# Kernel tuning notes

Hardware: AMD Instinct MI355X
Metric: run time of the kernel (lower is better)

Reference implementation:

```python
import jax, jax.numpy as jnp
import numpy as np

HEADS, DHEAD = 8, 32
INNER = HEADS * DHEAD  # 256


def _conv3x3(x, w, b):
    y = jax.lax.conv_general_dilated(x, w, (1, 1), ((1, 1), (1, 1)),
                                     dimension_numbers=('NCHW', 'OIHW', 'NCHW'))
    return y + b[None, :, None, None]


def _conv1x1(x, w, b):
    return jnp.einsum('oc,bchw->bohw', w, x) + b[None, :, None, None]


def setup_inputs() -> dict:
    key = jax.random.key(0)
    ks = jax.random.split(key, 16)
    s = 0.02
    return {
        'x': jax.random.normal(ks[0], (2, 256, 48, 48), jnp.float32),
        'luma': jax.random.uniform(ks[1], (2, 1, 48, 48), jnp.float32),
        'w_qkv': jax.random.normal(ks[2], (768, 256), jnp.float32) * s,
        'b_qkv': jax.random.normal(ks[3], (768,), jnp.float32) * s,
        'w_proj': jax.random.normal(ks[4], (256, 256), jnp.float32) * s,
        'b_proj': jax.random.normal(ks[5], (256,), jnp.float32) * s,
        'w_c1': jax.random.normal(ks[6], (128, 1, 3, 3), jnp.float32) * s,
        'b_c1': jax.random.normal(ks[7], (128,), jnp.float32) * s,
        'w_c2': jax.random.normal(ks[8], (128, 128, 3, 3), jnp.float32) * s,
        'b_c2': jax.random.normal(ks[9], (128,), jnp.float32) * s,
        'w_g': jax.random.normal(ks[10], (256, 128), jnp.float32) * s,
        'b_g': jax.random.normal(ks[11], (256,), jnp.float32) * s,
        'w_bt': jax.random.normal(ks[12], (256, 128), jnp.float32) * s,
        'b_bt': jax.random.normal(ks[13], (256,), jnp.float32) * s,
        'alpha': jax.random.normal(ks[14], (), jnp.float32) * 0.1,
    }


def reference(x, luma, w_qkv, b_qkv, w_proj, b_proj, w_c1, b_c1, w_c2, b_c2,
              w_g, b_g, w_bt, b_bt, alpha):
    B, C, H, W = x.shape
    N = H * W
    scale = DHEAD ** -0.5

    def to_heads(t):  # [B, h*d, H, W] -> [B, h, N, d]
        return t.reshape(B, HEADS, DHEAD, N).transpose(0, 1, 3, 2)

    qkv = _conv1x1(x, w_qkv, b_qkv)
    q = to_heads(qkv[:, 0 * INNER:1 * INNER])
    k = to_heads(qkv[:, 1 * INNER:2 * INNER])
    v = to_heads(qkv[:, 2 * INNER:3 * INNER])

    # luma conditioning net
    h = jax.nn.relu(_conv3x3(luma, w_c1, b_c1))
    h = jax.nn.relu(_conv3x3(h, w_c2, b_c2))
    gamma = to_heads(_conv1x1(h, w_g, b_g))
    beta = to_heads(_conv1x1(h, w_bt, b_bt))
    q = gamma * q + beta
    k = gamma * k + beta
    v = gamma * v + beta

    # luminance bias: avg_pool2d(3, stride=1, pad=1, count_include_pad=True)
    invL = 1.0 - luma
    invL = jax.lax.reduce_window(invL, 0.0, jax.lax.add, (1, 1, 3, 3), (1, 1, 1, 1),
                                 ((0, 0), (0, 0), (1, 1), (1, 1))) / 9.0
    invL = invL.reshape(B, N)
    invL = invL - invL.mean(axis=-1, keepdims=True)
    q = q + alpha * invL[:, None, :, None]

    attn = jax.nn.softmax(jnp.einsum('bhid,bhjd->bhij', q, k) * scale, axis=-1)
    out = jnp.einsum('bhij,bhjd->bhid', attn, v)
    out = out.transpose(0, 1, 3, 2).reshape(B, INNER, H, W)
    return _conv1x1(out, w_proj, b_proj)
```

## Files before the change

### kernel.cpp

```cpp
#include <hip/hip_runtime.h>
#include <hip/hip_bf16.h>
#include <math.h>
#include <string.h>

#define NB 2
#define NN 2304
#define NHEADS 8
#define DH 32
#define KPW 576

typedef __attribute__((ext_vector_type(8))) short v8s;
typedef __attribute__((ext_vector_type(4))) float v4f;

__device__ inline unsigned short f2b(float f) {
    unsigned u = __builtin_bit_cast(unsigned, f);
    unsigned r = u + 0x7FFFu + ((u >> 16) & 1u);
    return (unsigned short)(r >> 16);
}
__device__ inline float b2f(short s) {
    unsigned u = ((unsigned)(unsigned short)s) << 16;
    return __builtin_bit_cast(float, u);
}
__device__ inline unsigned pk2(float a, float b) {
    __hip_bfloat162 h = __float22bfloat162_rn(make_float2(a, b));
    unsigned r;
    memcpy(&r, &h, sizeof(r));
    return r;
}
__device__ inline float blo(unsigned u) { return __builtin_bit_cast(float, u << 16); }
__device__ inline float bhi(unsigned u) { return __builtin_bit_cast(float, u & 0xffff0000u); }

__global__ void k_prep(const float* __restrict__ wc1, const float* __restrict__ wc2,
                       const float* __restrict__ wqkv, const float* __restrict__ wg,
                       const float* __restrict__ wbt, const float* __restrict__ wproj,
                       float* __restrict__ twc1, short* __restrict__ tc2b,
                       short* __restrict__ wqkvb, short* __restrict__ wgb,
                       short* __restrict__ wbtb, short* __restrict__ wprojb,
                       float* __restrict__ vsum) {
    int i = blockIdx.x * 256 + threadIdx.x;
    if (i < 16 * DH) vsum[i] = 0.f;
    if (i < 9 * 128) {
        int k = i / 128, c = i % 128;
        twc1[i] = wc1[c * 9 + k];
    }
    if (i < 9 * 128 * 128) {
        int s = i / (128 * 128);
        int rem = i % (128 * 128);
        int o = rem / 128, ic = rem % 128;
        tc2b[i] = (short)f2b(wc2[(o * 128 + ic) * 9 + s]);
    }
    if (i < 768 * 256) wqkvb[i] = (short)f2b(wqkv[i]);
    if (i < 256 * 128) { wgb[i] = (short)f2b(wg[i]); wbtb[i] = (short)f2b(wbt[i]); }
    if (i < 256 * 256) wprojb[i] = (short)f2b(wproj[i]);
}

__global__ void k_front(const float* __restrict__ x, short* __restrict__ xt,
                        const float* __restrict__ luma, float* __restrict__ invl,
                        const float* __restrict__ twc1, const float* __restrict__ bc1,
                        short* __restrict__ h1p) {
    __shared__ unsigned short lds[64 * 66];
    __shared__ float red[256];
    int blk = blockIdx.x;
    if (blk >= NB * 144 + NB) {
        int cb = blk - (NB * 144 + NB);
        int c = threadIdx.x & 127;
        int p = (cb % 1250) * 2 + (threadIdx.x >> 7);
        int b = cb / 1250;
        int py = p / 50, px = p % 50;
        float val = 0.f;
        if (py >= 1 && py <= 48 && px >= 1 && px <= 48) {
            int y = py - 1, xx0 = px - 1;
            const float* lb = luma + b * NN;
            float acc = bc1[c];
#pragma unroll
            for (int ky = 0; ky < 3; ++ky) {
                int yy = y + ky - 1;
                if (yy < 0 || yy >= 48) continue;
#pragma unroll
                for (int kx = 0; kx < 3; ++kx) {
                    int xx = xx0 + kx - 1;
                    if (xx < 0 || xx >= 48) continue;
                    acc += twc1[(ky * 3 + kx) * 128 + c] * lb[yy * 48 + xx];
                }
            }
            val = fmaxf(acc, 0.f);
        }
        h1p[((size_t)b * 2500 + p) * 128 + c] = (short)f2b(val);
        return;
    }
    if (blk >= NB * 144) {
        int b = blk - NB * 144;
        const float* lb = luma + b * NN;
        float pooled[9];
        float local = 0.f;
#pragma unroll
        for (int it = 0; it < 9; ++it) {
            int n = it * 256 + threadIdx.x;
            int y = n / 48, xx0 = n % 48;
            float s = 0.f;
            for (int ky = 0; ky < 3; ++ky) {
                int yy = y + ky - 1;
                if (yy < 0 || yy >= 48) continue;
                for (int kx = 0; kx < 3; ++kx) {
                    int xx = xx0 + kx - 1;
                    if (xx < 0 || xx >= 48) continue;
                    s += 1.f - lb[yy * 48 + xx];
                }
            }
            s *= (1.f / 9.f);
            pooled[it] = s;
            local += s;
        }
        red[threadIdx.x] = local;
        __syncthreads();
        for (int off = 128; off > 0; off >>= 1) {
            if (threadIdx.x < off) red[threadIdx.x] += red[threadIdx.x + off];
            __syncthreads();
        }
        float mean = red[0] * (1.f / NN);
#pragma unroll
        for (int it = 0; it < 9; ++it) {
            int n = it * 256 + threadIdx.x;
            invl[b * NN + n] = pooled[it] - mean;
        }
        return;
    }
    int nt = blk % 36, ct = (blk / 36) % 4, b = blk / 144;
    int n0 = nt * 64, c0 = ct * 64;
    int nc = threadIdx.x & 63, cr = threadIdx.x >> 6;
#pragma unroll
    for (int i = 0; i < 16; ++i) {
        int cs = i * 4 + cr;
        float v = x[((size_t)b * 256 + c0 + cs) * NN + n0 + nc];
        lds[nc * 66 + cs] = f2b(v);
    }
    __syncthreads();
    int cc = threadIdx.x & 31, nr = threadIdx.x >> 5;
    unsigned* xt2 = (unsigned*)xt;
#pragma unroll
    for (int j = 0; j < 8; ++j) {
        int ns = j * 8 + nr;
        unsigned w = *(unsigned*)&lds[ns * 66 + 2 * cc];
        xt2[(((size_t)b * NN + n0 + ns) * 256 + c0) / 2 + cc] = w;
    }
}

__global__ __launch_bounds__(64) void k_conv2m(const short* __restrict__ h1p,
                                               const short* __restrict__ tc2b,
                                               const float* __restrict__ bc2,
                                               short* __restrict__ h2t) {
    int lane = threadIdx.x, l15 = lane & 15, g = lane >> 4;
    int blk = blockIdx.x;
    int ntg = blk % 36, ot = (blk / 36) % 8, b = blk / (36 * 8);
    int p0[4], na[4];
#pragma unroll
    for (int j = 0; j < 4; ++j) {
        int nt = ntg * 4 + j;
        int y = nt / 3, xx = (nt % 3) * 16;
        p0[j] = (y + 1) * 50 + xx + 1;
        na[j] = y * 48 + xx + l15;
    }
    const short* hb = h1p + (size_t)b * 2500 * 128;

    v4f acc[4] = {{0.f,0.f,0.f,0.f},{0.f,0.f,0.f,0.f},{0.f,0.f,0.f,0.f},{0.f,0.f,0.f,0.f}};
#pragma unroll
    for (int s = 0; s < 9; ++s) {
        int dp = (s / 3 - 1) * 50 + (s % 3 - 1);
#pragma unroll
        for (int kk = 0; kk < 4; ++kk) {
            v8s A = *(const v8s*)(tc2b + ((size_t)(s * 128 + ot * 16 + l15)) * 128 + kk * 32 + 8 * g);
#pragma unroll
            for (int j = 0; j < 4; ++j) {
                v8s B = *(const v8s*)(hb + (size_t)(p0[j] + dp + l15) * 128 + kk * 32 + 8 * g);
                acc[j] = __builtin_amdgcn_mfma_f32_16x16x32_bf16(A, B, acc[j], 0, 0, 0);
            }
        }
    }
    v4f bias = *(const v4f*)&bc2[ot * 16 + 4 * g];
#pragma unroll
    for (int j = 0; j < 4; ++j) {
        uint2 w;
        w.x = pk2(fmaxf(acc[j][0] + bias[0], 0.f), fmaxf(acc[j][1] + bias[1], 0.f));
        w.y = pk2(fmaxf(acc[j][2] + bias[2], 0.f), fmaxf(acc[j][3] + bias[3], 0.f));
        *(uint2*)&h2t[((size_t)b * NN + na[j]) * 128 + ot * 16 + 4 * g] = w;
    }
}

__global__ __launch_bounds__(64) void k_gbm(const short* __restrict__ h2t,
                                            const short* __restrict__ wgb,
                                            const short* __restrict__ wbtb,
                                            const float* __restrict__ bg,
                                            const float* __restrict__ bbt,
                                            short* __restrict__ gtb, short* __restrict__ bttb) {
    int lane = threadIdx.x, l15 = lane & 15, g = lane >> 4;
    int blk = blockIdx.x;
    int ntg = blk % 36, ot = (blk / 36) % 16, b = blk / (36 * 16);
    int n0 = ntg * 64;
    const short* hb = h2t + (size_t)b * NN * 128;

    v4f ga[4] = {{0.f,0.f,0.f,0.f},{0.f,0.f,0.f,0.f},{0.f,0.f,0.f,0.f},{0.f,0.f,0.f,0.f}};
    v4f ta[4] = {{0.f,0.f,0.f,0.f},{0.f,0.f,0.f,0.f},{0.f,0.f,0.f,0.f},{0.f,0.f,0.f,0.f}};
#pragma unroll
    for (int kk = 0; kk < 4; ++kk) {
        v8s Ag = *(const v8s*)(wgb + (size_t)(ot * 16 + l15) * 128 + kk * 32 + 8 * g);
        v8s At = *(const v8s*)(wbtb + (size_t)(ot * 16 + l15) * 128 + kk * 32 + 8 * g);
#pragma unroll
        for (int j = 0; j < 4; ++j) {
            v8s B = *(const v8s*)(hb + (size_t)(n0 + j * 16 + l15) * 128 + kk * 32 + 8 * g);
            ga[j] = __builtin_amdgcn_mfma_f32_16x16x32_bf16(Ag, B, ga[j], 0, 0, 0);
            ta[j] = __builtin_amdgcn_mfma_f32_16x16x32_bf16(At, B, ta[j], 0, 0, 0);
        }
    }
    v4f bgv = *(const v4f*)&bg[ot * 16 + 4 * g];
    v4f bbv = *(const v4f*)&bbt[ot * 16 + 4 * g];
#pragma unroll
    for (int j = 0; j < 4; ++j) {
        size_t o = ((size_t)b * NN + n0 + j * 16 + l15) * 256 + ot * 16 + 4 * g;
        uint2 w;
        w.x = pk2(ga[j][0] + bgv[0], ga[j][1] + bgv[1]);
        w.y = pk2(ga[j][2] + bgv[2], ga[j][3] + bgv[3]);
        *(uint2*)&gtb[o] = w;
        w.x = pk2(ta[j][0] + bbv[0], ta[j][1] + bbv[1]);
        w.y = pk2(ta[j][2] + bbv[2], ta[j][3] + bbv[3]);
        *(uint2*)&bttb[o] = w;
    }
}

__global__ __launch_bounds__(64) void k_qkvm(const short* __restrict__ xt,
                                             const short* __restrict__ wqkvb,
                                             const float* __restrict__ bqkv,
                                             const short* __restrict__ gtb,
                                             const short* __restrict__ bttb,
                                             const float* __restrict__ invl,
                                             const float* __restrict__ alpha_p,
                                             short* __restrict__ qb, short* __restrict__ kb,
                                             short* __restrict__ vraw) {
    int lane = threadIdx.x, l15 = lane & 15, g = lane >> 4;
    int blk = blockIdx.x;
    int ntg = blk % 36, otg = (blk / 36) % 24, b = blk / (36 * 24);
    int n0 = ntg * 64;
    const short* xb = xt + (size_t)b * NN * 256;

    v4f acc[2][4];
#pragma unroll
    for (int oa = 0; oa < 2; ++oa)
#pragma unroll
        for (int j = 0; j < 4; ++j) acc[oa][j] = (v4f){0.f, 0.f, 0.f, 0.f};
#pragma unroll
    for (int kk = 0; kk < 8; ++kk) {
        v8s A0 = *(const v8s*)(wqkvb + (size_t)(otg * 32 + l15) * 256 + kk * 32 + 8 * g);
        v8s A1 = *(const v8s*)(wqkvb + (size_t)(otg * 32 + 16 + l15) * 256 + kk * 32 + 8 * g);
#pragma unroll
        for (int j = 0; j < 4; ++j) {
            v8s B = *(const v8s*)(xb + (size_t)(n0 + j * 16 + l15) * 256 + kk * 32 + 8 * g);
            acc[0][j] = __builtin_amdgcn_mfma_f32_16x16x32_bf16(A0, B, acc[0][j], 0, 0, 0);
            acc[1][j] = __builtin_amdgcn_mfma_f32_16x16x32_bf16(A1, B, acc[1][j], 0, 0, 0);
        }
    }
    const float scale = 0.25503486f;
    float alpha = *alpha_p;
#pragma unroll
    for (int oa = 0; oa < 2; ++oa) {
        int ocb = otg * 32 + oa * 16;
        int which = ocb >> 8;
        int cbase = (ocb & 255) + 4 * g;
        int h = cbase >> 5, dbase = cbase & 31;
        v4f bias = *(const v4f*)&bqkv[ocb + 4 * g];
        short* dst = (which == 0) ? qb : (which == 1) ? kb : vraw;
#pragma unroll
        for (int j = 0; j < 4; ++j) {
            int n = n0 + j * 16 + l15;
            v4f a = acc[oa][j];
            uint2 gg = *(const uint2*)&gtb[((size_t)b * NN + n) * 256 + cbase];
            uint2 tt = *(const uint2*)&bttb[((size_t)b * NN + n) * 256 + cbase];
            float iv = (which == 0) ? alpha * invl[b * NN + n] : 0.f;
            float v0 = blo(gg.x) * (a[0] + bias[0]) + blo(tt.x);
            float v1 = bhi(gg.x) * (a[1] + bias[1]) + bhi(tt.x);
            float v2 = blo(gg.y) * (a[2] + bias[2]) + blo(tt.y);
            float v3 = bhi(gg.y) * (a[3] + bias[3]) + bhi(tt.y);
            if (which == 0) {
                v0 = (v0 + iv) * scale; v1 = (v1 + iv) * scale;
                v2 = (v2 + iv) * scale; v3 = (v3 + iv) * scale;
            }
            uint2 w;
            w.x = pk2(v0, v1);
            w.y = pk2(v2, v3);
            *(uint2*)&dst[(((size_t)b * NHEADS + h) * NN + n) * DH + dbase] = w;
        }
    }
}

__global__ void k_vt(const short* __restrict__ vraw, short* __restrict__ vtb,
                     float* __restrict__ vsum) {
    __shared__ unsigned short lds[64 * 34];
    int bh = blockIdx.x / 36, nc = blockIdx.x % 36;
    int n0 = nc * 64;
    int dpair = threadIdx.x & 15, nsub = (threadIdx.x >> 4) & 15;
    const unsigned* vr2 = (const unsigned*)vraw;
#pragma unroll
    for (int i = 0; i < 4; ++i) {
        int ns = i * 16 + nsub;
        unsigned v = vr2[((size_t)bh * NN + n0 + ns) * 16 + dpair];
        *(unsigned*)&lds[ns * 34 + 2 * dpair] = v;
    }
    __syncthreads();
    int pn = threadIdx.x & 31, drow = threadIdx.x >> 5;
    int kb0 = n0 >> 5;
    unsigned* vtb2 = (unsigned*)vtb;
#pragma unroll
    for (int j = 0; j < 4; ++j) {
        int d = j * 8 + drow;
        unsigned lo = lds[(2 * pn) * 34 + d];
        unsigned hi = lds[(2 * pn + 1) * 34 + d];
        vtb2[(((size_t)bh * 72 + kb0 + (pn >> 4)) * 32 + d) * 16 + (pn & 15)] = lo | (hi << 16);
    }
    if (threadIdx.x < 32) {
        int d = threadIdx.x;
        float s = 0.f;
        for (int ns = 0; ns < 64; ++ns) s += b2f((short)lds[ns * 34 + d]);
        atomicAdd(&vsum[bh * DH + d], s);
    }
}

__global__ __launch_bounds__(256) void k_attn2(const short* __restrict__ qb,
                                               const short* __restrict__ kbuf,
                                               const short* __restrict__ vtb,
                                               const float* __restrict__ vsum,
                                               short* __restrict__ aotb) {
    __shared__ short plds[4][64 * 40];
    __shared__ float acc_lds[4][64][35];
    __shared__ float ps_lds[4][64];
    int tid = threadIdx.x;
    int w = tid >> 6, lane = tid & 63;
    int l15 = lane & 15, g = lane >> 4;
    int blk = blockIdx.x;
    int logical = (blk & 7) * 72 + (blk >> 3);
    int qt = logical % 36, bh = logical / 36;
    int qbase = qt * 64;

    const short* qp = qb + ((size_t)bh * NN + qbase) * DH;
    const short* kp = kbuf + ((size_t)bh * NN + w * KPW) * DH;
    const short* vp = vtb + ((size_t)bh * 72 + w * (KPW / 32)) * 1024;

    v8s q0 = *(const v8s*)(qp + l15 * DH + 8 * g);
    v8s q1 = *(const v8s*)(qp + (16 + l15) * DH + 8 * g);
    v8s q2 = *(const v8s*)(qp + (32 + l15) * DH + 8 * g);
    v8s q3 = *(const v8s*)(qp + (48 + l15) * DH + 8 * g);

    const short one_b = (short)0x3F80;
    const v8s ones = {one_b, one_b, one_b, one_b, one_b, one_b, one_b, one_b};

    v4f acc[2][4];
#pragma unroll
    for (int dt = 0; dt < 2; ++dt)
#pragma unroll
        for (int qf = 0; qf < 4; ++qf) acc[dt][qf] = (v4f){0.f, 0.f, 0.f, 0.f};
    v4f ps[4] = {{0.f,0.f,0.f,0.f},{0.f,0.f,0.f,0.f},{0.f,0.f,0.f,0.f},{0.f,0.f,0.f,0.f}};
    short* pw = plds[w];

    for (int it = 0; it < KPW / 32; ++it) {
        const short* kpi = kp + it * 32 * DH;
        v8s ka0 = *(const v8s*)(kpi + l15 * DH + 8 * g);
        v8s ka1 = *(const v8s*)(kpi + (16 + l15) * DH + 8 * g);
        v4f s00 = __builtin_amdgcn_mfma_f32_16x16x32_bf16(ka0, q0, (v4f){0.f,0.f,0.f,0.f}, 0, 0, 0);
        v4f s01 = __builtin_amdgcn_mfma_f32_16x16x32_bf16(ka0, q1, (v4f){0.f,0.f,0.f,0.f}, 0, 0, 0);
        v4f s02 = __builtin_amdgcn_mfma_f32_16x16x32_bf16(ka0, q2, (v4f){0.f,0.f,0.f,0.f}, 0, 0, 0);
        v4f s03 = __builtin_amdgcn_mfma_f32_16x16x32_bf16(ka0, q3, (v4f){0.f,0.f,0.f,0.f}, 0, 0, 0);
        v4f s10 = __builtin_amdgcn_mfma_f32_16x16x32_bf16(ka1, q0, (v4f){0.f,0.f,0.f,0.f}, 0, 0, 0);
        v4f s11 = __builtin_amdgcn_mfma_f32_16x16x32_bf16(ka1, q1, (v4f){0.f,0.f,0.f,0.f}, 0, 0, 0);
        v4f s12 = __builtin_amdgcn_mfma_f32_16x16x32_bf16(ka1, q2, (v4f){0.f,0.f,0.f,0.f}, 0, 0, 0);
        v4f s13 = __builtin_amdgcn_mfma_f32_16x16x32_bf16(ka1, q3, (v4f){0.f,0.f,0.f,0.f}, 0, 0, 0);

#define DOFRAG(S, QF, KT)                                                        \
        {                                                                        \
            float p0 = __builtin_amdgcn_exp2f((S)[0]) - 1.f;                     \
            float p1 = __builtin_amdgcn_exp2f((S)[1]) - 1.f;                     \
            float p2 = __builtin_amdgcn_exp2f((S)[2]) - 1.f;                     \
            float p3 = __builtin_amdgcn_exp2f((S)[3]) - 1.f;                     \
            uint2 wv;                                                            \
            wv.x = pk2(p0, p1);                                                  \
            wv.y = pk2(p2, p3);                                                  \
            *(uint2*)((char*)pw + ((QF) * 16 + l15) * 80 + ((KT) * 16 + 4 * g) * 2) = wv; \
        }
        DOFRAG(s00, 0, 0)
        DOFRAG(s01, 1, 0)
        DOFRAG(s02, 2, 0)
        DOFRAG(s03, 3, 0)
        DOFRAG(s10, 0, 1)
        DOFRAG(s11, 1, 1)
        DOFRAG(s12, 2, 1)
        DOFRAG(s13, 3, 1)
#undef DOFRAG
        v8s pa0 = *(v8s*)((char*)pw + l15 * 80 + 16 * g);
        v8s pa1 = *(v8s*)((char*)pw + (16 + l15) * 80 + 16 * g);
        v8s pa2 = *(v8s*)((char*)pw + (32 + l15) * 80 + 16 * g);
        v8s pa3 = *(v8s*)((char*)pw + (48 + l15) * 80 + 16 * g);
        const short* vpi = vp + it * 1024;
        v8s vb0 = *(const v8s*)(vpi + l15 * 32 + 8 * g);
        v8s vb1 = *(const v8s*)(vpi + (16 + l15) * 32 + 8 * g);
        __builtin_amdgcn_s_setprio(1);
        acc[0][0] = __builtin_amdgcn_mfma_f32_16x16x32_bf16(pa0, vb0, acc[0][0], 0, 0, 0);
        acc[1][0] = __builtin_amdgcn_mfma_f32_16x16x32_bf16(pa0, vb1, acc[1][0], 0, 0, 0);
        acc[0][1] = __builtin_amdgcn_mfma_f32_16x16x32_bf16(pa1, vb0, acc[0][1], 0, 0, 0);
        acc[1][1] = __builtin_amdgcn_mfma_f32_16x16x32_bf16(pa1, vb1, acc[1][1], 0, 0, 0);
        acc[0][2] = __builtin_amdgcn_mfma_f32_16x16x32_bf16(pa2, vb0, acc[0][2], 0, 0, 0);
        acc[1][2] = __builtin_amdgcn_mfma_f32_16x16x32_bf16(pa2, vb1, acc[1][2], 0, 0, 0);
        acc[0][3] = __builtin_amdgcn_mfma_f32_16x16x32_bf16(pa3, vb0, acc[0][3], 0, 0, 0);
        acc[1][3] = __builtin_amdgcn_mfma_f32_16x16x32_bf16(pa3, vb1, acc[1][3], 0, 0, 0);
        ps[0] = __builtin_amdgcn_mfma_f32_16x16x32_bf16(pa0, ones, ps[0], 0, 0, 0);
        ps[1] = __builtin_amdgcn_mfma_f32_16x16x32_bf16(pa1, ones, ps[1], 0, 0, 0);
        ps[2] = __builtin_amdgcn_mfma_f32_16x16x32_bf16(pa2, ones, ps[2], 0, 0, 0);
        ps[3] = __builtin_amdgcn_mfma_f32_16x16x32_bf16(pa3, ones, ps[3], 0, 0, 0);
        __builtin_amdgcn_s_setprio(0);
    }

    if (l15 == 0) {
#pragma unroll
        for (int qf = 0; qf < 4; ++qf)
#pragma unroll
            for (int r = 0; r < 4; ++r)
                ps_lds[w][qf * 16 + 4 * g + r] = ps[qf][r];
    }
#pragma unroll
    for (int qf = 0; qf < 4; ++qf)
#pragma unroll
        for (int dt = 0; dt < 2; ++dt)
#pragma unroll
            for (int r = 0; r < 4; ++r)
                acc_lds[w][qf * 16 + 4 * g + r][dt * 16 + l15] = acc[dt][qf][r];
    __syncthreads();

    int q = tid >> 2, d0 = (tid & 3) * 8;
    float L = (float)NN;
    float a[8] = {0.f, 0.f, 0.f, 0.f, 0.f, 0.f, 0.f, 0.f};
#pragma unroll
    for (int wv = 0; wv < 4; ++wv) {
        L += ps_lds[wv][q];
        const float* row = &acc_lds[wv][q][d0];
#pragma unroll
        for (int j = 0; j < 8; ++j) a[j] += row[j];
    }
    const float* vs = vsum + bh * DH + d0;
    float rl = 1.f / L;
    uint4 o;
    o.x = pk2((a[0] + vs[0]) * rl, (a[1] + vs[1]) * rl);
    o.y = pk2((a[2] + vs[2]) * rl, (a[3] + vs[3]) * rl);
    o.z = pk2((a[4] + vs[4]) * rl, (a[5] + vs[5]) * rl);
    o.w = pk2((a[6] + vs[6]) * rl, (a[7] + vs[7]) * rl);
    int b = bh >> 3, h = bh & 7;
    *(uint4*)&aotb[((size_t)b * NN + qbase + q) * 256 + h * DH + d0] = o;
}

__global__ __launch_bounds__(64) void k_projm(const short* __restrict__ aotb,
                                              const short* __restrict__ wprojb,
                                              const float* __restrict__ bproj,
                                              float* __restrict__ out) {
    int lane = threadIdx.x, l15 = lane & 15, g = lane >> 4;
    int blk = blockIdx.x;
    int ntg = blk % 36, otg = (blk / 36) % 8, b = blk / (36 * 8);
    int n0 = ntg * 64;
    const short* ab = aotb + (size_t)b * NN * 256;

    v4f acc[2][4];
#pragma unroll
    for (int oa = 0; oa < 2; ++oa)
#pragma unroll
        for (int j = 0; j < 4; ++j) acc[oa][j] = (v4f){0.f, 0.f, 0.f, 0.f};
#pragma unroll
    for (int kk = 0; kk < 8; ++kk) {
        v8s A0 = *(const v8s*)(wprojb + (size_t)(otg * 32 + l15) * 256 + kk * 32 + 8 * g);
        v8s A1 = *(const v8s*)(wprojb + (size_t)(otg * 32 + 16 + l15) * 256 + kk * 32 + 8 * g);
#pragma unroll
        for (int j = 0; j < 4; ++j) {
            v8s B = *(const v8s*)(ab + (size_t)(n0 + j * 16 + l15) * 256 + kk * 32 + 8 * g);
            acc[0][j] = __builtin_amdgcn_mfma_f32_16x16x32_bf16(A0, B, acc[0][j], 0, 0, 0);
            acc[1][j] = __builtin_amdgcn_mfma_f32_16x16x32_bf16(A1, B, acc[1][j], 0, 0, 0);
        }
    }
#pragma unroll
    for (int oa = 0; oa < 2; ++oa) {
        v4f bias = *(const v4f*)&bproj[otg * 32 + oa * 16 + 4 * g];
#pragma unroll
        for (int j = 0; j < 4; ++j) {
#pragma unroll
            for (int r = 0; r < 4; ++r) {
                int o = otg * 32 + oa * 16 + 4 * g + r;
                out[((size_t)b * 256 + o) * NN + n0 + j * 16 + l15] = acc[oa][j][r] + bias[r];
            }
        }
    }
}

extern "C" void kernel_launch(void* const* d_in, const int* in_sizes, int n_in,
                              void* d_out, int out_size, void* d_ws, size_t ws_size,
                              hipStream_t stream) {
    const float* x     = (const float*)d_in[0];
    const float* luma  = (const float*)d_in[1];
    const float* wqkv  = (const float*)d_in[2];
    const float* bqkv  = (const float*)d_in[3];
    const float* wproj = (const float*)d_in[4];
    const float* bproj = (const float*)d_in[5];
    const float* wc1   = (const float*)d_in[6];
    const float* bc1   = (const float*)d_in[7];
    const float* wc2   = (const float*)d_in[8];
    const float* bc2   = (const float*)d_in[9];
    const float* wg    = (const float*)d_in[10];
    const float* bg    = (const float*)d_in[11];
    const float* wbt   = (const float*)d_in[12];
    const float* bbt   = (const float*)d_in[13];
    const float* alpha = (const float*)d_in[14];
    float* out = (float*)d_out;

    float* ws = (float*)d_ws;
    size_t off = 0;
    float* twc1 = ws + off;            off += 9 * 128;
    short* tc2b = (short*)(ws + off);  off += 9 * 128 * 128 / 2;
    short* wqkvb = (short*)(ws + off); off += 768 * 256 / 2;
    short* wgb = (short*)(ws + off);   off += 256 * 128 / 2;
    short* wbtb = (short*)(ws + off);  off += 256 * 128 / 2;
    short* wprojb = (short*)(ws + off); off += 256 * 256 / 2;
    short* h1p = (short*)(ws + off);   off += NB * 2500 * 128 / 2;
    short* xt = (short*)(ws + off);    off += NB * NN * 256 / 2;
    short* h2t = (short*)(ws + off);   off += NB * NN * 128 / 2;
    short* gtb = (short*)(ws + off);   off += NB * NN * 256 / 2;
    short* bttb = (short*)(ws + off);  off += NB * NN * 256 / 2;
    float* invl = ws + off;            off += NB * NN;
    short* qbb = (short*)(ws + off);   off += 16 * NN * DH / 2;
    short* kbb = (short*)(ws + off);   off += 16 * NN * DH / 2;
    short* vraw = (short*)(ws + off);  off += 16 * NN * DH / 2;
    short* vtb = (short*)(ws + off);   off += 16 * NN * DH / 2;
    float* vsum = ws + off;            off += 16 * DH;
    short* aotb = (short*)(ws + off);  off += NB * NN * 256 / 2;
    (void)ws_size; (void)in_sizes; (void)n_in; (void)out_size;

    k_prep<<<768, 256, 0, stream>>>(wc1, wc2, wqkv, wg, wbt, wproj,
                                    twc1, tc2b, wqkvb, wgb, wbtb, wprojb, vsum);
    k_front<<<NB * 144 + NB + NB * 1250, 256, 0, stream>>>(x, xt, luma, invl, twc1, bc1, h1p);
    k_conv2m<<<NB * 8 * 36, 64, 0, stream>>>(h1p, tc2b, bc2, h2t);
    k_gbm<<<NB * 16 * 36, 64, 0, stream>>>(h2t, wgb, wbtb, bg, bbt, gtb, bttb);
    k_qkvm<<<NB * 24 * 36, 64, 0, stream>>>(xt, wqkvb, bqkv, gtb, bttb, invl, alpha,
                                            qbb, kbb, vraw);
    k_vt<<<16 * 36, 256, 0, stream>>>(vraw, vtb, vsum);
    k_attn2<<<576, 256, 0, stream>>>(qbb, kbb, vtb, vsum, aotb);
    k_projm<<<NB * 8 * 36, 64, 0, stream>>>(aotb, wprojb, bproj, out);
}
```

Measured before the change: 111.0 us.

## Split attention into 32-query tiles with 8 key-split waves per block

The attention kernel now gives each block 32 queries instead of 64 and splits the keys across 8 waves of 288 keys rather than 4 waves of 576. Grid and block sizes double, which raises parallelism and shortens each wave's serial loop. The cross-wave partial sums now pass through LDS as bf16 instead of fp32, which shrinks shared memory but adds rounding error. Q-fragment reuse per K/V load is halved, so global K/V traffic per query roughly doubles.

New measurement: 98.57 us. -11.2%, faster.

```diff
diff --git a/kernel.cpp b/kernel.cpp
--- a/kernel.cpp
+++ b/kernel.cpp
@@ -7,7 +7,8 @@
 #define NN 2304
 #define NHEADS 8
 #define DH 32
-#define KPW 576
+#define AW 8
+#define KPW 288
 
 typedef __attribute__((ext_vector_type(8))) short v8s;
 typedef __attribute__((ext_vector_type(4))) float v4f;
@@ -322,21 +323,21 @@
     }
 }
 
-__global__ __launch_bounds__(256) void k_attn2(const short* __restrict__ qb,
+__global__ __launch_bounds__(512) void k_attn2(const short* __restrict__ qb,
                                                const short* __restrict__ kbuf,
                                                const short* __restrict__ vtb,
                                                const float* __restrict__ vsum,
                                                short* __restrict__ aotb) {
-    __shared__ short plds[4][64 * 40];
-    __shared__ float acc_lds[4][64][35];
-    __shared__ float ps_lds[4][64];
+    __shared__ short plds[AW][32 * 40];
+    __shared__ short acch[AW][32][33];
+    __shared__ float ps_lds[AW][32];
     int tid = threadIdx.x;
     int w = tid >> 6, lane = tid & 63;
     int l15 = lane & 15, g = lane >> 4;
     int blk = blockIdx.x;
-    int logical = (blk & 7) * 72 + (blk >> 3);
-    int qt = logical % 36, bh = logical / 36;
-    int qbase = qt * 64;
+    int logical = (blk & 7) * 144 + (blk >> 3);
+    int qt = logical % 72, bh = logical / 72;
+    int qbase = qt * 32;
 
     const short* qp = qb + ((size_t)bh * NN + qbase) * DH;
     const short* kp = kbuf + ((size_t)bh * NN + w * KPW) * DH;
@@ -344,18 +345,12 @@
 
     v8s q0 = *(const v8s*)(qp + l15 * DH + 8 * g);
     v8s q1 = *(const v8s*)(qp + (16 + l15) * DH + 8 * g);
-    v8s q2 = *(const v8s*)(qp + (32 + l15) * DH + 8 * g);
-    v8s q3 = *(const v8s*)(qp + (48 + l15) * DH + 8 * g);
 
     const short one_b = (short)0x3F80;
     const v8s ones = {one_b, one_b, one_b, one_b, one_b, one_b, one_b, one_b};
 
-    v4f acc[2][4];
-#pragma unroll
-    for (int dt = 0; dt < 2; ++dt)
-#pragma unroll
-        for (int qf = 0; qf < 4; ++qf) acc[dt][qf] = (v4f){0.f, 0.f, 0.f, 0.f};
-    v4f ps[4] = {{0.f,0.f,0.f,0.f},{0.f,0.f,0.f,0.f},{0.f,0.f,0.f,0.f},{0.f,0.f,0.f,0.f}};
+    v4f acc00 = {0.f,0.f,0.f,0.f}, acc01 = acc00, acc10 = acc00, acc11 = acc00;
+    v4f ps0 = {0.f,0.f,0.f,0.f}, ps1 = ps0;
     short* pw = plds[w];
 
     for (int it = 0; it < KPW / 32; ++it) {
@@ -364,12 +359,8 @@
         v8s ka1 = *(const v8s*)(kpi + (16 + l15) * DH + 8 * g);
         v4f s00 = __builtin_amdgcn_mfma_f32_16x16x32_bf16(ka0, q0, (v4f){0.f,0.f,0.f,0.f}, 0, 0, 0);
         v4f s01 = __builtin_amdgcn_mfma_f32_16x16x32_bf16(ka0, q1, (v4f){0.f,0.f,0.f,0.f}, 0, 0, 0);
-        v4f s02 = __builtin_amdgcn_mfma_f32_16x16x32_bf16(ka0, q2, (v4f){0.f,0.f,0.f,0.f}, 0, 0, 0);
-        v4f s03 = __builtin_amdgcn_mfma_f32_16x16x32_bf16(ka0, q3, (v4f){0.f,0.f,0.f,0.f}, 0, 0, 0);
         v4f s10 = __builtin_amdgcn_mfma_f32_16x16x32_bf16(ka1, q0, (v4f){0.f,0.f,0.f,0.f}, 0, 0, 0);
         v4f s11 = __builtin_amdgcn_mfma_f32_16x16x32_bf16(ka1, q1, (v4f){0.f,0.f,0.f,0.f}, 0, 0, 0);
-        v4f s12 = __builtin_amdgcn_mfma_f32_16x16x32_bf16(ka1, q2, (v4f){0.f,0.f,0.f,0.f}, 0, 0, 0);
-        v4f s13 = __builtin_amdgcn_mfma_f32_16x16x32_bf16(ka1, q3, (v4f){0.f,0.f,0.f,0.f}, 0, 0, 0);
 
 #define DOFRAG(S, QF, KT)                                                        \
         {                                                                        \
@@ -384,71 +375,54 @@
         }
         DOFRAG(s00, 0, 0)
         DOFRAG(s01, 1, 0)
-        DOFRAG(s02, 2, 0)
-        DOFRAG(s03, 3, 0)
         DOFRAG(s10, 0, 1)
         DOFRAG(s11, 1, 1)
-        DOFRAG(s12, 2, 1)
-        DOFRAG(s13, 3, 1)
 #undef DOFRAG
         v8s pa0 = *(v8s*)((char*)pw + l15 * 80 + 16 * g);
         v8s pa1 = *(v8s*)((char*)pw + (16 + l15) * 80 + 16 * g);
-        v8s pa2 = *(v8s*)((char*)pw + (32 + l15) * 80 + 16 * g);
-        v8s pa3 = *(v8s*)((char*)pw + (48 + l15) * 80 + 16 * g);
         const short* vpi = vp + it * 1024;
         v8s vb0 = *(const v8s*)(vpi + l15 * 32 + 8 * g);
         v8s vb1 = *(const v8s*)(vpi + (16 + l15) * 32 + 8 * g);
         __builtin_amdgcn_s_setprio(1);
-        acc[0][0] = __builtin_amdgcn_mfma_f32_16x16x32_bf16(pa0, vb0, acc[0][0], 0, 0, 0);
-        acc[1][0] = __builtin_amdgcn_mfma_f32_16x16x32_bf16(pa0, vb1, acc[1][0], 0, 0, 0);
-        acc[0][1] = __builtin_amdgcn_mfma_f32_16x16x32_bf16(pa1, vb0, acc[0][1], 0, 0, 0);
-        acc[1][1] = __builtin_amdgcn_mfma_f32_16x16x32_bf16(pa1, vb1, acc[1][1], 0, 0, 0);
-        acc[0][2] = __builtin_amdgcn_mfma_f32_16x16x32_bf16(pa2, vb0, acc[0][2], 0, 0, 0);
-        acc[1][2] = __builtin_amdgcn_mfma_f32_16x16x32_bf16(pa2, vb1, acc[1][2], 0, 0, 0);
-        acc[0][3] = __builtin_amdgcn_mfma_f32_16x16x32_bf16(pa3, vb0, acc[0][3], 0, 0, 0);
-        acc[1][3] = __builtin_amdgcn_mfma_f32_16x16x32_bf16(pa3, vb1, acc[1][3], 0, 0, 0);
-        ps[0] = __builtin_amdgcn_mfma_f32_16x16x32_bf16(pa0, ones, ps[0], 0, 0, 0);
-        ps[1] = __builtin_amdgcn_mfma_f32_16x16x32_bf16(pa1, ones, ps[1], 0, 0, 0);
-        ps[2] = __builtin_amdgcn_mfma_f32_16x16x32_bf16(pa2, ones, ps[2], 0, 0, 0);
-        ps[3] = __builtin_amdgcn_mfma_f32_16x16x32_bf16(pa3, ones, ps[3], 0, 0, 0);
+        acc00 = __builtin_amdgcn_mfma_f32_16x16x32_bf16(pa0, vb0, acc00, 0, 0, 0);
+        acc01 = __builtin_amdgcn_mfma_f32_16x16x32_bf16(pa0, vb1, acc01, 0, 0, 0);
+        acc10 = __builtin_amdgcn_mfma_f32_16x16x32_bf16(pa1, vb0, acc10, 0, 0, 0);
+        acc11 = __builtin_amdgcn_mfma_f32_16x16x32_bf16(pa1, vb1, acc11, 0, 0, 0);
+        ps0 = __builtin_amdgcn_mfma_f32_16x16x32_bf16(pa0, ones, ps0, 0, 0, 0);
+        ps1 = __builtin_amdgcn_mfma_f32_16x16x32_bf16(pa1, ones, ps1, 0, 0, 0);
         __builtin_amdgcn_s_setprio(0);
     }
 
     if (l15 == 0) {
 #pragma unroll
-        for (int qf = 0; qf < 4; ++qf)
-#pragma unroll
-            for (int r = 0; r < 4; ++r)
-                ps_lds[w][qf * 16 + 4 * g + r] = ps[qf][r];
-    }
-#pragma unroll
-    for (int qf = 0; qf < 4; ++qf)
-#pragma unroll
-        for (int dt = 0; dt < 2; ++dt)
-#pragma unroll
-            for (int r = 0; r < 4; ++r)
-                acc_lds[w][qf * 16 + 4 * g + r][dt * 16 + l15] = acc[dt][qf][r];
+        for (int r = 0; r < 4; ++r) {
+            ps_lds[w][4 * g + r] = ps0[r];
+            ps_lds[w][16 + 4 * g + r] = ps1[r];
+        }
+    }
+#pragma unroll
+    for (int r = 0; r < 4; ++r) {
+        acch[w][4 * g + r][l15]      = (short)f2b(acc00[r]);
+        acch[w][4 * g + r][16 + l15] = (short)f2b(acc01[r]);
+        acch[w][16 + 4 * g + r][l15]      = (short)f2b(acc10[r]);
+        acch[w][16 + 4 * g + r][16 + l15] = (short)f2b(acc11[r]);
+    }
     __syncthreads();
 
-    int q = tid >> 2, d0 = (tid & 3) * 8;
+    int q = tid >> 4, d0 = (tid & 15) * 2;
     float L = (float)NN;
-    float a[8] = {0.f, 0.f, 0.f, 0.f, 0.f, 0.f, 0.f, 0.f};
-#pragma unroll
-    for (int wv = 0; wv < 4; ++wv) {
+    float a0 = 0.f, a1 = 0.f;
+#pragma unroll
+    for (int wv = 0; wv < AW; ++wv) {
         L += ps_lds[wv][q];
-        const float* row = &acc_lds[wv][q][d0];
-#pragma unroll
-        for (int j = 0; j < 8; ++j) a[j] += row[j];
+        a0 += b2f(acch[wv][q][d0]);
+        a1 += b2f(acch[wv][q][d0 + 1]);
     }
     const float* vs = vsum + bh * DH + d0;
     float rl = 1.f / L;
-    uint4 o;
-    o.x = pk2((a[0] + vs[0]) * rl, (a[1] + vs[1]) * rl);
-    o.y = pk2((a[2] + vs[2]) * rl, (a[3] + vs[3]) * rl);
-    o.z = pk2((a[4] + vs[4]) * rl, (a[5] + vs[5]) * rl);
-    o.w = pk2((a[6] + vs[6]) * rl, (a[7] + vs[7]) * rl);
+    unsigned o = pk2((a0 + vs[0]) * rl, (a1 + vs[1]) * rl);
     int b = bh >> 3, h = bh & 7;
-    *(uint4*)&aotb[((size_t)b * NN + qbase + q) * 256 + h * DH + d0] = o;
+    *(unsigned*)&aotb[((size_t)b * NN + qbase + q) * 256 + h * DH + d0] = o;
 }
 
 __global__ __launch_bounds__(64) void k_projm(const short* __restrict__ aotb,
@@ -541,6 +515,6 @@
     k_qkvm<<<NB * 24 * 36, 64, 0, stream>>>(xt, wqkvb, bqkv, gtb, bttb, invl, alpha,
                                             qbb, kbb, vraw);
     k_vt<<<16 * 36, 256, 0, stream>>>(vraw, vtb, vsum);
-    k_attn2<<<576, 256, 0, stream>>>(qbb, kbb, vtb, vsum, aotb);
+    k_attn2<<<1152, 512, 0, stream>>>(qbb, kbb, vtb, vsum, aotb);
     k_projm<<<NB * 8 * 36, 64, 0, stream>>>(aotb, wprojb, bproj, out);
 }
```

## Fold weight prep into front kernel and split attention keys over eight waves

Applied to the files above, without the earlier changes.

Weight conversion to bf16 now runs as extra blocks of the front kernel, and the conv1 weights are read directly instead of through a transposed copy. This removes one kernel launch and its serialization. The attention kernel now uses 8 waves (512 threads), each covering 288 keys instead of 576, which doubles parallelism within a block. The per-wave partial accumulators are stored in LDS as bf16 so the larger wave count still fits in shared memory. That adds rounding error to the partial sums before they are reduced.

Result: faster. 98.71 us (-11.1%).

```diff
diff --git a/kernel.cpp b/kernel.cpp
--- a/kernel.cpp
+++ b/kernel.cpp
@@ -7,7 +7,8 @@
 #define NN 2304
 #define NHEADS 8
 #define DH 32
-#define KPW 576
+#define AW 8
+#define KPW 288
 
 typedef __attribute__((ext_vector_type(8))) short v8s;
 typedef __attribute__((ext_vector_type(4))) float v4f;
@@ -30,39 +31,38 @@
 __device__ inline float blo(unsigned u) { return __builtin_bit_cast(float, u << 16); }
 __device__ inline float bhi(unsigned u) { return __builtin_bit_cast(float, u & 0xffff0000u); }
 
-__global__ void k_prep(const float* __restrict__ wc1, const float* __restrict__ wc2,
-                       const float* __restrict__ wqkv, const float* __restrict__ wg,
-                       const float* __restrict__ wbt, const float* __restrict__ wproj,
-                       float* __restrict__ twc1, short* __restrict__ tc2b,
-                       short* __restrict__ wqkvb, short* __restrict__ wgb,
-                       short* __restrict__ wbtb, short* __restrict__ wprojb,
-                       float* __restrict__ vsum) {
-    int i = blockIdx.x * 256 + threadIdx.x;
-    if (i < 16 * DH) vsum[i] = 0.f;
-    if (i < 9 * 128) {
-        int k = i / 128, c = i % 128;
-        twc1[i] = wc1[c * 9 + k];
-    }
-    if (i < 9 * 128 * 128) {
-        int s = i / (128 * 128);
-        int rem = i % (128 * 128);
-        int o = rem / 128, ic = rem % 128;
-        tc2b[i] = (short)f2b(wc2[(o * 128 + ic) * 9 + s]);
-    }
-    if (i < 768 * 256) wqkvb[i] = (short)f2b(wqkv[i]);
-    if (i < 256 * 128) { wgb[i] = (short)f2b(wg[i]); wbtb[i] = (short)f2b(wbt[i]); }
-    if (i < 256 * 256) wprojb[i] = (short)f2b(wproj[i]);
-}
-
 __global__ void k_front(const float* __restrict__ x, short* __restrict__ xt,
                         const float* __restrict__ luma, float* __restrict__ invl,
-                        const float* __restrict__ twc1, const float* __restrict__ bc1,
-                        short* __restrict__ h1p) {
+                        const float* __restrict__ wc1, const float* __restrict__ bc1,
+                        short* __restrict__ h1p,
+                        const float* __restrict__ wc2, const float* __restrict__ wqkv,
+                        const float* __restrict__ wg, const float* __restrict__ wbt,
+                        const float* __restrict__ wproj,
+                        short* __restrict__ tc2b, short* __restrict__ wqkvb,
+                        short* __restrict__ wgb, short* __restrict__ wbtb,
+                        short* __restrict__ wprojb, float* __restrict__ vsum) {
     __shared__ unsigned short lds[64 * 66];
     __shared__ float red[256];
     int blk = blockIdx.x;
-    if (blk >= NB * 144 + NB) {
-        int cb = blk - (NB * 144 + NB);
+    const int XT_END = NB * 144;
+    const int INVL_END = XT_END + NB;
+    const int CONV1_END = INVL_END + NB * 1250;
+    if (blk >= CONV1_END) {
+        int i = (blk - CONV1_END) * 256 + threadIdx.x;
+        if (i < 16 * DH) vsum[i] = 0.f;
+        if (i < 9 * 128 * 128) {
+            int s = i / (128 * 128);
+            int rem = i % (128 * 128);
+            int o = rem / 128, ic = rem % 128;
+            tc2b[i] = (short)f2b(wc2[(o * 128 + ic) * 9 + s]);
+        }
+        if (i < 768 * 256) wqkvb[i] = (short)f2b(wqkv[i]);
+        if (i < 256 * 128) { wgb[i] = (short)f2b(wg[i]); wbtb[i] = (short)f2b(wbt[i]); }
+        if (i < 256 * 256) wprojb[i] = (short)f2b(wproj[i]);
+        return;
+    }
+    if (blk >= INVL_END) {
+        int cb = blk - INVL_END;
         int c = threadIdx.x & 127;
         int p = (cb % 1250) * 2 + (threadIdx.x >> 7);
         int b = cb / 1250;
@@ -80,7 +80,7 @@
                 for (int kx = 0; kx < 3; ++kx) {
                     int xx = xx0 + kx - 1;
                     if (xx < 0 || xx >= 48) continue;
-                    acc += twc1[(ky * 3 + kx) * 128 + c] * lb[yy * 48 + xx];
+                    acc += wc1[c * 9 + ky * 3 + kx] * lb[yy * 48 + xx];
                 }
             }
             val = fmaxf(acc, 0.f);
@@ -88,8 +88,8 @@
         h1p[((size_t)b * 2500 + p) * 128 + c] = (short)f2b(val);
         return;
     }
-    if (blk >= NB * 144) {
-        int b = blk - NB * 144;
+    if (blk >= XT_END) {
+        int b = blk - XT_END;
         const float* lb = luma + b * NN;
         float pooled[9];
         float local = 0.f;
@@ -322,14 +322,14 @@
     }
 }
 
-__global__ __launch_bounds__(256) void k_attn2(const short* __restrict__ qb,
+__global__ __launch_bounds__(512) void k_attn2(const short* __restrict__ qb,
                                                const short* __restrict__ kbuf,
                                                const short* __restrict__ vtb,
                                                const float* __restrict__ vsum,
                                                short* __restrict__ aotb) {
-    __shared__ short plds[4][64 * 40];
-    __shared__ float acc_lds[4][64][35];
-    __shared__ float ps_lds[4][64];
+    __shared__ short plds[AW][64 * 40];
+    __shared__ short acch[AW][64][36];
+    __shared__ float ps_lds[AW][64];
     int tid = threadIdx.x;
     int w = tid >> 6, lane = tid & 63;
     int l15 = lane & 15, g = lane >> 4;
@@ -424,31 +424,28 @@
 #pragma unroll
     for (int qf = 0; qf < 4; ++qf)
 #pragma unroll
-        for (int dt = 0; dt < 2; ++dt)
-#pragma unroll
-            for (int r = 0; r < 4; ++r)
-                acc_lds[w][qf * 16 + 4 * g + r][dt * 16 + l15] = acc[dt][qf][r];
+        for (int r = 0; r < 4; ++r) {
+            acch[w][qf * 16 + 4 * g + r][l15]      = (short)f2b(acc[0][qf][r]);
+            acch[w][qf * 16 + 4 * g + r][16 + l15] = (short)f2b(acc[1][qf][r]);
+        }
     __syncthreads();
 
-    int q = tid >> 2, d0 = (tid & 3) * 8;
+    int q = tid >> 3, d0 = (tid & 7) * 4;
     float L = (float)NN;
-    float a[8] = {0.f, 0.f, 0.f, 0.f, 0.f, 0.f, 0.f, 0.f};
-#pragma unroll
-    for (int wv = 0; wv < 4; ++wv) {
+    float a0 = 0.f, a1 = 0.f, a2 = 0.f, a3 = 0.f;
+#pragma unroll
+    for (int wv = 0; wv < AW; ++wv) {
         L += ps_lds[wv][q];
-        const float* row = &acc_lds[wv][q][d0];
-#pragma unroll
-        for (int j = 0; j < 8; ++j) a[j] += row[j];
+        const short* row = &acch[wv][q][d0];
+        a0 += b2f(row[0]); a1 += b2f(row[1]); a2 += b2f(row[2]); a3 += b2f(row[3]);
     }
     const float* vs = vsum + bh * DH + d0;
     float rl = 1.f / L;
-    uint4 o;
-    o.x = pk2((a[0] + vs[0]) * rl, (a[1] + vs[1]) * rl);
-    o.y = pk2((a[2] + vs[2]) * rl, (a[3] + vs[3]) * rl);
-    o.z = pk2((a[4] + vs[4]) * rl, (a[5] + vs[5]) * rl);
-    o.w = pk2((a[6] + vs[6]) * rl, (a[7] + vs[7]) * rl);
+    uint2 o;
+    o.x = pk2((a0 + vs[0]) * rl, (a1 + vs[1]) * rl);
+    o.y = pk2((a2 + vs[2]) * rl, (a3 + vs[3]) * rl);
     int b = bh >> 3, h = bh & 7;
-    *(uint4*)&aotb[((size_t)b * NN + qbase + q) * 256 + h * DH + d0] = o;
+    *(uint2*)&aotb[((size_t)b * NN + qbase + q) * 256 + h * DH + d0] = o;
 }
 
 __global__ __launch_bounds__(64) void k_projm(const short* __restrict__ aotb,
@@ -513,7 +510,6 @@
 
     float* ws = (float*)d_ws;
     size_t off = 0;
-    float* twc1 = ws + off;            off += 9 * 128;
     short* tc2b = (short*)(ws + off);  off += 9 * 128 * 128 / 2;
     short* wqkvb = (short*)(ws + off); off += 768 * 256 / 2;
     short* wgb = (short*)(ws + off);   off += 256 * 128 / 2;
@@ -533,14 +529,15 @@
     short* aotb = (short*)(ws + off);  off += NB * NN * 256 / 2;
     (void)ws_size; (void)in_sizes; (void)n_in; (void)out_size;
 
-    k_prep<<<768, 256, 0, stream>>>(wc1, wc2, wqkv, wg, wbt, wproj,
-                                    twc1, tc2b, wqkvb, wgb, wbtb, wprojb, vsum);
-    k_front<<<NB * 144 + NB + NB * 1250, 256, 0, stream>>>(x, xt, luma, invl, twc1, bc1, h1p);
+    int front_grid = NB * 144 + NB + NB * 1250 + 768;
+    k_front<<<front_grid, 256, 0, stream>>>(x, xt, luma, invl, wc1, bc1, h1p,
+                                            wc2, wqkv, wg, wbt, wproj,
+                                            tc2b, wqkvb, wgb, wbtb, wprojb, vsum);
     k_conv2m<<<NB * 8 * 36, 64, 0, stream>>>(h1p, tc2b, bc2, h2t);
     k_gbm<<<NB * 16 * 36, 64, 0, stream>>>(h2t, wgb, wbtb, bg, bbt, gtb, bttb);
     k_qkvm<<<NB * 24 * 36, 64, 0, stream>>>(xt, wqkvb, bqkv, gtb, bttb, invl, alpha,
                                             qbb, kbb, vraw);
     k_vt<<<16 * 36, 256, 0, stream>>>(vraw, vtb, vsum);
-    k_attn2<<<576, 256, 0, stream>>>(qbb, kbb, vtb, vsum, aotb);
+    k_attn2<<<576, 512, 0, stream>>>(qbb, kbb, vtb, vsum, aotb);
     k_projm<<<NB * 8 * 36, 64, 0, stream>>>(aotb, wprojb, bproj, out);
 }
```
